# Optimization experiments

Measured on AMD Instinct MI355X. Metric: run time of the kernel, lower is better.

Reference implementation:

```python
import jax, jax.numpy as jnp
import numpy as np
from functools import partial

B, T, D, H, K = 4, 2048, 256, 8, 31
HD = D // H
EXP = 2  # FeedForward expansion
EPS = 1e-5


def setup_inputs() -> dict:
    key = jax.random.key(0)
    ks = iter(jax.random.split(key, 32))
    s = 0.02
    n = lambda shape: jax.random.normal(next(ks), shape, jnp.float32) * s
    ones = lambda shape: jnp.ones(shape, jnp.float32)
    zeros = lambda shape: jnp.zeros(shape, jnp.float32)
    return {
        "x": jax.random.normal(next(ks), (B, T, D), jnp.float32),
        # FF1
        "ff1_ln_g": ones((D,)), "ff1_ln_b": zeros((D,)),
        "ff1_w1": n((D, D * EXP)), "ff1_b1": zeros((D * EXP,)),
        "ff1_w2": n((D * EXP, D)), "ff1_b2": zeros((D,)),
        # MHSA
        "mhsa_ln_g": ones((D,)), "mhsa_ln_b": zeros((D,)),
        "qkv_w": n((D, 3 * D)), "qkv_b": zeros((3 * D,)),
        "out_w": n((D, D)), "out_b": zeros((D,)),
        # Conv module
        "conv_ln_g": ones((D,)), "conv_ln_b": zeros((D,)),
        "pw1_w": n((D, 2 * D)), "pw1_b": zeros((2 * D,)),
        "dw_w": n((D, 1, K)), "dw_b": zeros((D,)),
        "bn_g": ones((D,)), "bn_b": zeros((D,)),
        "pw2_w": n((D, D)), "pw2_b": zeros((D,)),
        # FF2
        "ff2_ln_g": ones((D,)), "ff2_ln_b": zeros((D,)),
        "ff2_w1": n((D, D * EXP)), "ff2_b1": zeros((D * EXP,)),
        "ff2_w2": n((D * EXP, D)), "ff2_b2": zeros((D,)),
        # Final LN
        "final_ln_g": ones((D,)), "final_ln_b": zeros((D,)),
    }


def layer_norm(x, g, b):
    mu = jnp.mean(x, axis=-1, keepdims=True)
    var = jnp.mean(jnp.square(x - mu), axis=-1, keepdims=True)
    return (x - mu) * jax.lax.rsqrt(var + EPS) * g + b


def feed_forward(x, ln_g, ln_b, w1, b1, w2, b2):
    h = layer_norm(x, ln_g, ln_b)
    h = jax.nn.silu(h @ w1 + b1)
    h = h @ w2 + b2
    return x + 0.5 * h


def mhsa(x, ln_g, ln_b, qkv_w, qkv_b, out_w, out_b):
    Bc, Tc, C = x.shape
    h = layer_norm(x, ln_g, ln_b)
    qkv = (h @ qkv_w + qkv_b).reshape(Bc, Tc, 3, H, HD)
    qkv = jnp.transpose(qkv, (2, 0, 3, 1, 4))  # [3,B,H,T,hd]
    q, k, v = qkv[0], qkv[1], qkv[2]
    attn = jnp.einsum("bhqd,bhkd->bhqk", q, k) / jnp.sqrt(jnp.float32(HD))
    attn = jax.nn.softmax(attn, axis=-1)
    out = jnp.einsum("bhqk,bhkd->bhqd", attn, v)
    out = jnp.transpose(out, (0, 2, 1, 3)).reshape(Bc, Tc, C)
    return x + (out @ out_w + out_b)


def conv_module(x, ln_g, ln_b, pw1_w, pw1_b, dw_w, dw_b, bn_g, bn_b, pw2_w, pw2_b):
    h = layer_norm(x, ln_g, ln_b)
    h = h @ pw1_w + pw1_b                      # [B,T,2D]
    a, g = jnp.split(h, 2, axis=-1)
    h = a * jax.nn.sigmoid(g)                  # GLU -> [B,T,D]
    h = jnp.transpose(h, (0, 2, 1))            # [B,D,T]
    h = jax.lax.conv_general_dilated(
        h, dw_w, window_strides=(1,), padding=[(K // 2, K // 2)],
        dimension_numbers=("NCH", "OIH", "NCH"), feature_group_count=D,
    ) + dw_b[None, :, None]
    # BatchNorm1d (training-mode batch stats, biased variance) over (B,T) per channel
    mu = jnp.mean(h, axis=(0, 2), keepdims=True)
    var = jnp.mean(jnp.square(h - mu), axis=(0, 2), keepdims=True)
    h = (h - mu) * jax.lax.rsqrt(var + EPS)
    h = h * bn_g[None, :, None] + bn_b[None, :, None]
    h = jax.nn.silu(h)
    h = jnp.transpose(h, (0, 2, 1))            # [B,T,D]
    h = h @ pw2_w + pw2_b
    return x + h


def reference(x,
              ff1_ln_g, ff1_ln_b, ff1_w1, ff1_b1, ff1_w2, ff1_b2,
              mhsa_ln_g, mhsa_ln_b, qkv_w, qkv_b, out_w, out_b,
              conv_ln_g, conv_ln_b, pw1_w, pw1_b, dw_w, dw_b, bn_g, bn_b,
              pw2_w, pw2_b,
              ff2_ln_g, ff2_ln_b, ff2_w1, ff2_b1, ff2_w2, ff2_b2,
              final_ln_g, final_ln_b):
    x = feed_forward(x, ff1_ln_g, ff1_ln_b, ff1_w1, ff1_b1, ff1_w2, ff1_b2)
    x = mhsa(x, mhsa_ln_g, mhsa_ln_b, qkv_w, qkv_b, out_w, out_b)
    x = conv_module(x, conv_ln_g, conv_ln_b, pw1_w, pw1_b, dw_w, dw_b,
                    bn_g, bn_b, pw2_w, pw2_b)
    x = feed_forward(x, ff2_ln_g, ff2_ln_b, ff2_w1, ff2_b1, ff2_w2, ff2_b2)
    return layer_norm(x, final_ln_g, final_ln_b)
```

## Files before the change

kernel.cpp:

```cpp
#include <hip/hip_runtime.h>
#include <hip/hip_bf16.h>

#define Bn 4
#define Tn 2048
#define Dn 256
#define Hn 8
#define HDn 32
#define KW 31
#define EPSV 1e-5f
#define NTOK (Bn * Tn)

typedef __attribute__((ext_vector_type(8))) short bf16x8;
typedef __attribute__((ext_vector_type(4))) float f32x4;
typedef unsigned short ushort_t;

__device__ __forceinline__ float sigmoidf_(float x) { return 1.f / (1.f + __expf(-x)); }
__device__ __forceinline__ unsigned short f2bfu(float f) {
    __hip_bfloat16 h = __float2bfloat16(f);
    unsigned short u; __builtin_memcpy(&u, &h, 2); return u;
}

template <int OUTBF>
__global__ __launch_bounds__(256) void ln_kernel(const float* __restrict__ x,
                                                 const float* __restrict__ g,
                                                 const float* __restrict__ b,
                                                 void* __restrict__ yp)
{
    const int row  = blockIdx.x * 4 + (threadIdx.x >> 6);
    const int lane = threadIdx.x & 63;
    const float* xr = x + (size_t)row * Dn + lane * 4;
    float4 v = *(const float4*)xr;
    float s = v.x + v.y + v.z + v.w;
#pragma unroll
    for (int o = 32; o > 0; o >>= 1) s += __shfl_xor(s, o, 64);
    const float mu = s * (1.f / Dn);
    const float dx = v.x - mu, dy = v.y - mu, dz = v.z - mu, dw = v.w - mu;
    float ss = dx * dx + dy * dy + dz * dz + dw * dw;
#pragma unroll
    for (int o = 32; o > 0; o >>= 1) ss += __shfl_xor(ss, o, 64);
    const float rstd = rsqrtf(ss * (1.f / Dn) + EPSV);
    const float4 gv = *(const float4*)(g + lane * 4);
    const float4 bv = *(const float4*)(b + lane * 4);
    float o0 = dx * rstd * gv.x + bv.x;
    float o1 = dy * rstd * gv.y + bv.y;
    float o2 = dz * rstd * gv.z + bv.z;
    float o3 = dw * rstd * gv.w + bv.w;
    if (OUTBF) {
        ushort4 o4;
        o4.x = f2bfu(o0); o4.y = f2bfu(o1); o4.z = f2bfu(o2); o4.w = f2bfu(o3);
        *(ushort4*)((ushort_t*)yp + (size_t)row * Dn + lane * 4) = o4;
    } else {
        float4 o4 = {o0, o1, o2, o3};
        *(float4*)((float*)yp + (size_t)row * Dn + lane * 4) = o4;
    }
}

struct WP {
    const float* s[8];
    unsigned     off[8];
    int          Kd[8];
    int          Nd[8];
};

__global__ __launch_bounds__(256) void wprep_kernel(WP p, ushort_t* __restrict__ wb)
{
    const int z = blockIdx.z;
    const int N = p.Nd[z], K = p.Kd[z];
    const int n0 = blockIdx.x * 64, k0 = blockIdx.y * 32;
    if (n0 >= N || k0 >= K) return;
    const float* src = p.s[z];
    ushort_t* dst = wb + p.off[z];
    const int nl = threadIdx.x & 63, kq = threadIdx.x >> 6;
    const int n = n0 + nl;
    const int kb = k0 + kq * 8;
    bf16x8 o;
#pragma unroll
    for (int i = 0; i < 8; ++i) o[i] = (short)f2bfu(src[(size_t)(kb + i) * N + n]);
    *(bf16x8*)(dst + (size_t)n * K + kb) = o;
}

template <int EPI>
__global__ __launch_bounds__(256) void bgemm_kernel(const ushort_t* __restrict__ A,
                                                    const ushort_t* __restrict__ Bt,
                                                    const float* __restrict__ bias,
                                                    const float* __restrict__ res,
                                                    void* __restrict__ Cp,
                                                    int N, int K, float scale)
{
    __shared__ ushort_t Af[8][64][8];
    __shared__ ushort_t Bf[8][64][8];
    const int tid = threadIdx.x;
    const int w   = tid >> 6;
    const int l   = tid & 63;
    const int g   = l >> 4;
    const int q16 = l & 15;
    const int wm  = w >> 1;
    const int wn  = w & 1;
    const int row0 = blockIdx.x * 128;
    const int col0 = blockIdx.y * 128;

    const ushort_t* ga0 = A  + (size_t)(row0 + (2 * w + 0) * 16 + q16) * K + g * 8;
    const ushort_t* ga1 = A  + (size_t)(row0 + (2 * w + 1) * 16 + q16) * K + g * 8;
    const ushort_t* gb0 = Bt + (size_t)(col0 + (2 * w + 0) * 16 + q16) * K + g * 8;
    const ushort_t* gb1 = Bt + (size_t)(col0 + (2 * w + 1) * 16 + q16) * K + g * 8;

    f32x4 acc[4][4];
#pragma unroll
    for (int mt = 0; mt < 4; ++mt)
#pragma unroll
        for (int nt = 0; nt < 4; ++nt) { acc[mt][nt].x = 0.f; acc[mt][nt].y = 0.f; acc[mt][nt].z = 0.f; acc[mt][nt].w = 0.f; }

    bf16x8 sa0 = *(const bf16x8*)ga0;
    bf16x8 sa1 = *(const bf16x8*)ga1;
    bf16x8 sb0 = *(const bf16x8*)gb0;
    bf16x8 sb1 = *(const bf16x8*)gb1;

    const int NKT = K >> 5;
    for (int kt = 0; kt < NKT; ++kt) {
        __syncthreads();
        *(bf16x8*)&Af[2 * w + 0][l][0] = sa0;
        *(bf16x8*)&Af[2 * w + 1][l][0] = sa1;
        *(bf16x8*)&Bf[2 * w + 0][l][0] = sb0;
        *(bf16x8*)&Bf[2 * w + 1][l][0] = sb1;
        if (kt + 1 < NKT) {
            const int k = (kt + 1) * 32;
            sa0 = *(const bf16x8*)(ga0 + k);
            sa1 = *(const bf16x8*)(ga1 + k);
            sb0 = *(const bf16x8*)(gb0 + k);
            sb1 = *(const bf16x8*)(gb1 + k);
        }
        __syncthreads();
        bf16x8 af[4], bb[4];
#pragma unroll
        for (int mt = 0; mt < 4; ++mt) af[mt] = *(const bf16x8*)&Af[wm * 4 + mt][l][0];
#pragma unroll
        for (int nt = 0; nt < 4; ++nt) bb[nt] = *(const bf16x8*)&Bf[wn * 4 + nt][l][0];
#pragma unroll
        for (int mt = 0; mt < 4; ++mt)
#pragma unroll
            for (int nt = 0; nt < 4; ++nt)
                acc[mt][nt] = __builtin_amdgcn_mfma_f32_16x16x32_bf16(af[mt], bb[nt], acc[mt][nt], 0, 0, 0);
    }

#pragma unroll
    for (int nt = 0; nt < 4; ++nt) {
        const int col = col0 + (wn * 4 + nt) * 16 + q16;
        const float bj = bias[col];
#pragma unroll
        for (int mt = 0; mt < 4; ++mt) {
            const int rowb = row0 + (wm * 4 + mt) * 16 + g * 4;
#pragma unroll
            for (int r = 0; r < 4; ++r) {
                float v = acc[mt][nt][r] + bj;
                const size_t idx = (size_t)(rowb + r) * N + col;
                if (EPI == 1) v *= sigmoidf_(v);
                if (EPI == 0 || EPI == 1) {
                    ((ushort_t*)Cp)[idx] = f2bfu(v);
                } else if (EPI == 2) {
                    ((float*)Cp)[idx] = res[idx] + scale * v;
                } else {
                    ((float*)Cp)[idx] = v;
                }
            }
        }
    }
}

__global__ __launch_bounds__(256) void attn_mfma_kernel(const ushort_t* __restrict__ qkv,
                                                        ushort_t* __restrict__ out)
{
    __shared__ ushort_t Kl[64][40];
    __shared__ ushort_t Vt[32][72];
    __shared__ ushort_t Pl[4][16][72];

    const int tid = threadIdx.x;
    const int w   = tid >> 6;
    const int l   = tid & 63;
    const int g   = l >> 4;
    const int q16 = l & 15;
    const int b   = blockIdx.y >> 3;
    const int h   = blockIdx.y & 7;
    const int q0  = blockIdx.x * 128 + w * 32;
    const ushort_t* base = qkv + (size_t)b * Tn * 768;

    bf16x8 qf[2];
#pragma unroll
    for (int u = 0; u < 2; ++u)
        qf[u] = *(const bf16x8*)(base + (size_t)(q0 + u * 16 + q16) * 768 + h * 32 + g * 8);

    f32x4 O[2][2];
    float mrun[2][4], lrun[2][4];
#pragma unroll
    for (int u = 0; u < 2; ++u)
#pragma unroll
        for (int t = 0; t < 2; ++t) { O[u][t].x = 0.f; O[u][t].y = 0.f; O[u][t].z = 0.f; O[u][t].w = 0.f; }
#pragma unroll
    for (int u = 0; u < 2; ++u)
#pragma unroll
        for (int r = 0; r < 4; ++r) { mrun[u][r] = 0.f; lrun[u][r] = 0.f; }

    const float cs = 0.25505392367033404f;

    const int kvr = tid >> 2;
    const int dsg = (tid & 3) * 8;

    for (int c0 = 0; c0 < Tn; c0 += 64) {
        __syncthreads();
        {
            const ushort_t* kp = base + (size_t)(c0 + kvr) * 768 + 256 + h * 32 + dsg;
            bf16x8 kk = *(const bf16x8*)kp;
            bf16x8 vv = *(const bf16x8*)(kp + 256);
            *(bf16x8*)&Kl[kvr][dsg] = kk;
            const int vcol = kvr ^ (dsg << 1);
#pragma unroll
            for (int i = 0; i < 8; ++i) Vt[dsg + i][vcol] = (ushort_t)vv[i];
        }
        __syncthreads();

        bf16x8 kb[4];
#pragma unroll
        for (int t = 0; t < 4; ++t)
            kb[t] = *(const bf16x8*)&Kl[t * 16 + q16][g * 8];
        bf16x8 vb[2][2];
#pragma unroll
        for (int ht = 0; ht < 2; ++ht) {
            const int d = ht * 16 + q16;
#pragma unroll
            for (int c = 0; c < 2; ++c)
                vb[ht][c] = *(const bf16x8*)&Vt[d][(c * 32 + g * 8) ^ ((d & 24) << 1)];
        }

#pragma unroll
        for (int u = 0; u < 2; ++u) {
            float p[4][4];
#pragma unroll
            for (int t = 0; t < 4; ++t) {
                f32x4 z = {0.f, 0.f, 0.f, 0.f};
                f32x4 s = __builtin_amdgcn_mfma_f32_16x16x32_bf16(qf[u], kb[t], z, 0, 0, 0);
#pragma unroll
                for (int r = 0; r < 4; ++r) p[t][r] = s[r] * cs;
            }
            float mx[4];
#pragma unroll
            for (int r = 0; r < 4; ++r)
                mx[r] = fmaxf(fmaxf(p[0][r], p[1][r]), fmaxf(p[2][r], p[3][r]));
#pragma unroll
            for (int o = 1; o < 16; o <<= 1)
#pragma unroll
                for (int r = 0; r < 4; ++r) mx[r] = fmaxf(mx[r], __shfl_xor(mx[r], o, 64));
            float wg = mx[0] - mrun[u][0];
#pragma unroll
            for (int r = 1; r < 4; ++r) wg = fmaxf(wg, mx[r] - mrun[u][r]);
            if (__any(wg > 11.f)) {
#pragma unroll
                for (int r = 0; r < 4; ++r) {
                    const float mn = fmaxf(mrun[u][r], mx[r]);
                    const float f  = exp2f(mrun[u][r] - mn);
                    lrun[u][r] *= f;
                    O[u][0][r] *= f;
                    O[u][1][r] *= f;
                    mrun[u][r] = mn;
                }
            }
#pragma unroll
            for (int t = 0; t < 4; ++t)
#pragma unroll
                for (int r = 0; r < 4; ++r) {
                    const float pe = exp2f(p[t][r] - mrun[u][r]);
                    lrun[u][r] += pe;
                    Pl[w][g * 4 + r][(t * 16 + q16) ^ (g << 4)] = f2bfu(pe);
                }
            bf16x8 pa[2];
#pragma unroll
            for (int c = 0; c < 2; ++c)
                pa[c] = *(const bf16x8*)&Pl[w][q16][(c * 32 + g * 8) ^ ((q16 >> 2) << 4)];
#pragma unroll
            for (int ht = 0; ht < 2; ++ht) {
                O[u][ht] = __builtin_amdgcn_mfma_f32_16x16x32_bf16(pa[0], vb[ht][0], O[u][ht], 0, 0, 0);
                O[u][ht] = __builtin_amdgcn_mfma_f32_16x16x32_bf16(pa[1], vb[ht][1], O[u][ht], 0, 0, 0);
            }
        }
    }

#pragma unroll
    for (int u = 0; u < 2; ++u) {
#pragma unroll
        for (int o = 1; o < 16; o <<= 1)
#pragma unroll
            for (int r = 0; r < 4; ++r) lrun[u][r] += __shfl_xor(lrun[u][r], o, 64);
#pragma unroll
        for (int r = 0; r < 4; ++r) {
            const float inv = 1.f / lrun[u][r];
            const int row = b * Tn + q0 + u * 16 + g * 4 + r;
#pragma unroll
            for (int ht = 0; ht < 2; ++ht)
                out[(size_t)row * Dn + h * 32 + ht * 16 + q16] = f2bfu(O[u][ht][r] * inv);
        }
    }
}

__global__ __launch_bounds__(256) void glu_kernel(const float* __restrict__ h,
                                                  float* __restrict__ outp)
{
    const size_t i   = (size_t)blockIdx.x * 256 + threadIdx.x;
    const size_t row = i / (Dn / 4);
    const int    c4  = (int)(i % (Dn / 4)) * 4;
    const float* hp  = h + row * (2 * Dn);
    const float4 a = *(const float4*)(hp + c4);
    const float4 g = *(const float4*)(hp + Dn + c4);
    float4 r;
    r.x = a.x * sigmoidf_(g.x);
    r.y = a.y * sigmoidf_(g.y);
    r.z = a.z * sigmoidf_(g.z);
    r.w = a.w * sigmoidf_(g.w);
    *(float4*)(outp + row * Dn + c4) = r;
}

__global__ __launch_bounds__(256) void dwconv_kernel(const float* __restrict__ in,
                                                     const float* __restrict__ w,
                                                     const float* __restrict__ wb,
                                                     float* __restrict__ outp)
{
    const int d  = threadIdx.x;
    const int b  = blockIdx.y;
    const int t0 = blockIdx.x * 8;
    float wr[KW];
#pragma unroll
    for (int k = 0; k < KW; ++k) wr[k] = w[d * KW + k];
    const float bias = wb[d];
    const float* bin  = in + (size_t)b * Tn * Dn + d;
    float* bout       = outp + (size_t)b * Tn * Dn + d;
    if (t0 >= (KW / 2) + 1 && t0 + 8 + KW / 2 <= Tn) {
        for (int i = 0; i < 8; ++i) {
            const int t = t0 + i;
            float s = bias;
#pragma unroll
            for (int k = 0; k < KW; ++k) s = fmaf(bin[(size_t)(t + k - KW / 2) * Dn], wr[k], s);
            bout[(size_t)t * Dn] = s;
        }
    } else {
        for (int i = 0; i < 8; ++i) {
            const int t = t0 + i;
            float s = bias;
#pragma unroll
            for (int k = 0; k < KW; ++k) {
                const int tt = t + k - KW / 2;
                if (tt >= 0 && tt < Tn) s = fmaf(bin[(size_t)tt * Dn], wr[k], s);
            }
            bout[(size_t)t * Dn] = s;
        }
    }
}

__global__ __launch_bounds__(256) void bnpart_kernel(const float* __restrict__ in,
                                                     float* __restrict__ part)
{
    const int d  = threadIdx.x;
    const int bk = blockIdx.x;
    float s = 0.f, ss = 0.f;
    const float* p = in + (size_t)bk * 32 * Dn + d;
    for (int t = 0; t < 32; ++t) {
        const float v = p[(size_t)t * Dn];
        s += v;
        ss = fmaf(v, v, ss);
    }
    part[bk * 512 + d]       = s;
    part[bk * 512 + 256 + d] = ss;
}

__global__ __launch_bounds__(256) void bnfin_kernel(const float* __restrict__ part,
                                                    float* __restrict__ meanp,
                                                    float* __restrict__ rstdp)
{
    const int d = threadIdx.x;
    float s = 0.f, ss = 0.f;
    for (int k = 0; k < 256; ++k) {
        s  += part[k * 512 + d];
        ss += part[k * 512 + 256 + d];
    }
    const float mu  = s * (1.f / NTOK);
    const float var = ss * (1.f / NTOK) - mu * mu;
    meanp[d] = mu;
    rstdp[d] = rsqrtf(var + EPSV);
}

__global__ __launch_bounds__(256) void bnsilu_kernel(const float* __restrict__ in,
                                                     const float* __restrict__ meanp,
                                                     const float* __restrict__ rstdp,
                                                     const float* __restrict__ g,
                                                     const float* __restrict__ bb,
                                                     ushort_t* __restrict__ outp)
{
    const size_t idx = ((size_t)blockIdx.x * 256 + threadIdx.x) * 4;
    const int d = (int)(idx & (Dn - 1));
    const float4 v = *(const float4*)(in + idx);
    ushort4 r;
    {
        float t;
        t = (v.x - meanp[d + 0]) * rstdp[d + 0] * g[d + 0] + bb[d + 0]; r.x = f2bfu(t * sigmoidf_(t));
        t = (v.y - meanp[d + 1]) * rstdp[d + 1] * g[d + 1] + bb[d + 1]; r.y = f2bfu(t * sigmoidf_(t));
        t = (v.z - meanp[d + 2]) * rstdp[d + 2] * g[d + 2] + bb[d + 2]; r.z = f2bfu(t * sigmoidf_(t));
        t = (v.w - meanp[d + 3]) * rstdp[d + 3] * g[d + 3] + bb[d + 3]; r.w = f2bfu(t * sigmoidf_(t));
    }
    *(ushort4*)(outp + idx) = r;
}

extern "C" void kernel_launch(void* const* d_in, const int* in_sizes, int n_in,
                              void* d_out, int out_size, void* d_ws, size_t ws_size,
                              hipStream_t stream)
{
    const float* x         = (const float*)d_in[0];
    const float* ff1_ln_g  = (const float*)d_in[1];
    const float* ff1_ln_b  = (const float*)d_in[2];
    const float* ff1_w1    = (const float*)d_in[3];
    const float* ff1_b1    = (const float*)d_in[4];
    const float* ff1_w2    = (const float*)d_in[5];
    const float* ff1_b2    = (const float*)d_in[6];
    const float* mhsa_ln_g = (const float*)d_in[7];
    const float* mhsa_ln_b = (const float*)d_in[8];
    const float* qkv_w     = (const float*)d_in[9];
    const float* qkv_b     = (const float*)d_in[10];
    const float* out_w     = (const float*)d_in[11];
    const float* out_b     = (const float*)d_in[12];
    const float* conv_ln_g = (const float*)d_in[13];
    const float* conv_ln_b = (const float*)d_in[14];
    const float* pw1_w     = (const float*)d_in[15];
    const float* pw1_b     = (const float*)d_in[16];
    const float* dw_w      = (const float*)d_in[17];
    const float* dw_b      = (const float*)d_in[18];
    const float* bn_g      = (const float*)d_in[19];
    const float* bn_b      = (const float*)d_in[20];
    const float* pw2_w     = (const float*)d_in[21];
    const float* pw2_b     = (const float*)d_in[22];
    const float* ff2_ln_g  = (const float*)d_in[23];
    const float* ff2_ln_b  = (const float*)d_in[24];
    const float* ff2_w1    = (const float*)d_in[25];
    const float* ff2_b1    = (const float*)d_in[26];
    const float* ff2_w2    = (const float*)d_in[27];
    const float* ff2_b2    = (const float*)d_in[28];
    const float* fin_ln_g  = (const float*)d_in[29];
    const float* fin_ln_b  = (const float*)d_in[30];

    char* W = (char*)d_ws;
    const size_t MB = 1u << 20;
    float*    R     = (float*)W;
    ushort_t* NbBF  = (ushort_t*)(W + 8 * MB);
    ushort_t* HBF   = (ushort_t*)(W + 12 * MB);
    float*    Hf32  = (float*)(W + 12 * MB);
    float*    Cb    = (float*)(W + 12 * MB);
    ushort_t* AtBF  = (ushort_t*)(W + 24 * MB);
    float*    part  = (float*)(W + 28 * MB);
    float*    meanp = part + 131072;
    float*    rstdp = meanp + 256;
    ushort_t* wbuf  = (ushort_t*)(W + 29 * MB);

    ushort_t* qkvT = wbuf;
    ushort_t* outT = wbuf + 196608;
    ushort_t* f11T = wbuf + 262144;
    ushort_t* f12T = wbuf + 393216;
    ushort_t* f21T = wbuf + 524288;
    ushort_t* f22T = wbuf + 655360;
    ushort_t* pw1T = wbuf + 786432;
    ushort_t* pw2T = wbuf + 917504;

    const dim3 blk(256);

    WP wp;
    wp.s[0] = qkv_w;  wp.off[0] = 0;      wp.Kd[0] = 256; wp.Nd[0] = 768;
    wp.s[1] = out_w;  wp.off[1] = 196608; wp.Kd[1] = 256; wp.Nd[1] = 256;
    wp.s[2] = ff1_w1; wp.off[2] = 262144; wp.Kd[2] = 256; wp.Nd[2] = 512;
    wp.s[3] = ff1_w2; wp.off[3] = 393216; wp.Kd[3] = 512; wp.Nd[3] = 256;
    wp.s[4] = ff2_w1; wp.off[4] = 524288; wp.Kd[4] = 256; wp.Nd[4] = 512;
    wp.s[5] = ff2_w2; wp.off[5] = 655360; wp.Kd[5] = 512; wp.Nd[5] = 256;
    wp.s[6] = pw1_w;  wp.off[6] = 786432; wp.Kd[6] = 256; wp.Nd[6] = 512;
    wp.s[7] = pw2_w;  wp.off[7] = 917504; wp.Kd[7] = 256; wp.Nd[7] = 256;
    wprep_kernel<<<dim3(12, 16, 8), blk, 0, stream>>>(wp, wbuf);

    ln_kernel<1><<<NTOK / 4, blk, 0, stream>>>(x, ff1_ln_g, ff1_ln_b, NbBF);
    bgemm_kernel<1><<<dim3(64, 4), blk, 0, stream>>>(NbBF, f11T, ff1_b1, nullptr, HBF, 512, 256, 0.f);
    bgemm_kernel<2><<<dim3(64, 2), blk, 0, stream>>>(HBF, f12T, ff1_b2, x, R, 256, 512, 0.5f);

    ln_kernel<1><<<NTOK / 4, blk, 0, stream>>>(R, mhsa_ln_g, mhsa_ln_b, NbBF);
    bgemm_kernel<0><<<dim3(64, 6), blk, 0, stream>>>(NbBF, qkvT, qkv_b, nullptr, HBF, 768, 256, 0.f);
    attn_mfma_kernel<<<dim3(16, 32), blk, 0, stream>>>(HBF, AtBF);
    bgemm_kernel<2><<<dim3(64, 2), blk, 0, stream>>>(AtBF, outT, out_b, R, R, 256, 256, 1.f);

    ln_kernel<1><<<NTOK / 4, blk, 0, stream>>>(R, conv_ln_g, conv_ln_b, NbBF);
    bgemm_kernel<3><<<dim3(64, 4), blk, 0, stream>>>(NbBF, pw1T, pw1_b, nullptr, Hf32, 512, 256, 0.f);
    glu_kernel<<<NTOK * Dn / 4 / 256, blk, 0, stream>>>(Hf32, (float*)d_out);
    dwconv_kernel<<<dim3(Tn / 8, Bn), blk, 0, stream>>>((float*)d_out, dw_w, dw_b, Cb);
    bnpart_kernel<<<256, blk, 0, stream>>>(Cb, part);
    bnfin_kernel<<<1, blk, 0, stream>>>(part, meanp, rstdp);
    bnsilu_kernel<<<NTOK * Dn / 4 / 256, blk, 0, stream>>>(Cb, meanp, rstdp, bn_g, bn_b, AtBF);
    bgemm_kernel<2><<<dim3(64, 2), blk, 0, stream>>>(AtBF, pw2T, pw2_b, R, R, 256, 256, 1.f);

    ln_kernel<1><<<NTOK / 4, blk, 0, stream>>>(R, ff2_ln_g, ff2_ln_b, NbBF);
    bgemm_kernel<1><<<dim3(64, 4), blk, 0, stream>>>(NbBF, f21T, ff2_b1, nullptr, HBF, 512, 256, 0.f);
    bgemm_kernel<2><<<dim3(64, 2), blk, 0, stream>>>(HBF, f22T, ff2_b2, R, R, 256, 512, 0.5f);

    ln_kernel<0><<<NTOK / 4, blk, 0, stream>>>(R, fin_ln_g, fin_ln_b, d_out);
}
```

Measured before the change: 392.8 us.

## Shrink GEMM tiles, per-wave K/V staging in attention, lazy softmax max

```diff
diff --git a/kernel.cpp b/kernel.cpp
--- a/kernel.cpp
+++ b/kernel.cpp
@@ -79,7 +79,7 @@
     *(bf16x8*)(dst + (size_t)n * K + kb) = o;
 }
 
-template <int EPI>
+template <int EPI, int BM>
 __global__ __launch_bounds__(256) void bgemm_kernel(const ushort_t* __restrict__ A,
                                                     const ushort_t* __restrict__ Bt,
                                                     const float* __restrict__ bias,
@@ -87,8 +87,11 @@
                                                     void* __restrict__ Cp,
                                                     int N, int K, float scale)
 {
-    __shared__ ushort_t Af[8][64][8];
-    __shared__ ushort_t Bf[8][64][8];
+    constexpr int ABLK = BM / 16;
+    constexpr int AST  = ABLK / 4;
+    constexpr int MT   = BM / 32;
+    __shared__ ushort_t Af[ABLK][64][8];
+    __shared__ ushort_t Bf[4][64][8];
     const int tid = threadIdx.x;
     const int w   = tid >> 6;
     const int l   = tid & 63;
@@ -96,59 +99,59 @@
     const int q16 = l & 15;
     const int wm  = w >> 1;
     const int wn  = w & 1;
-    const int row0 = blockIdx.x * 128;
-    const int col0 = blockIdx.y * 128;
-
-    const ushort_t* ga0 = A  + (size_t)(row0 + (2 * w + 0) * 16 + q16) * K + g * 8;
-    const ushort_t* ga1 = A  + (size_t)(row0 + (2 * w + 1) * 16 + q16) * K + g * 8;
-    const ushort_t* gb0 = Bt + (size_t)(col0 + (2 * w + 0) * 16 + q16) * K + g * 8;
-    const ushort_t* gb1 = Bt + (size_t)(col0 + (2 * w + 1) * 16 + q16) * K + g * 8;
-
-    f32x4 acc[4][4];
-#pragma unroll
-    for (int mt = 0; mt < 4; ++mt)
-#pragma unroll
-        for (int nt = 0; nt < 4; ++nt) { acc[mt][nt].x = 0.f; acc[mt][nt].y = 0.f; acc[mt][nt].z = 0.f; acc[mt][nt].w = 0.f; }
-
-    bf16x8 sa0 = *(const bf16x8*)ga0;
-    bf16x8 sa1 = *(const bf16x8*)ga1;
-    bf16x8 sb0 = *(const bf16x8*)gb0;
-    bf16x8 sb1 = *(const bf16x8*)gb1;
+    const int row0 = blockIdx.x * BM;
+    const int col0 = blockIdx.y * 64;
+    const int sbi  = tid >> 6;
+
+    const ushort_t* ga[AST];
+#pragma unroll
+    for (int i = 0; i < AST; ++i)
+        ga[i] = A + (size_t)(row0 + (sbi + 4 * i) * 16 + q16) * K + g * 8;
+    const ushort_t* gb = Bt + (size_t)(col0 + sbi * 16 + q16) * K + g * 8;
+
+    f32x4 acc[MT][2];
+#pragma unroll
+    for (int mt = 0; mt < MT; ++mt)
+#pragma unroll
+        for (int nt = 0; nt < 2; ++nt) { acc[mt][nt].x = 0.f; acc[mt][nt].y = 0.f; acc[mt][nt].z = 0.f; acc[mt][nt].w = 0.f; }
+
+    bf16x8 sa[AST], sb;
+#pragma unroll
+    for (int i = 0; i < AST; ++i) sa[i] = *(const bf16x8*)ga[i];
+    sb = *(const bf16x8*)gb;
 
     const int NKT = K >> 5;
     for (int kt = 0; kt < NKT; ++kt) {
         __syncthreads();
-        *(bf16x8*)&Af[2 * w + 0][l][0] = sa0;
-        *(bf16x8*)&Af[2 * w + 1][l][0] = sa1;
-        *(bf16x8*)&Bf[2 * w + 0][l][0] = sb0;
-        *(bf16x8*)&Bf[2 * w + 1][l][0] = sb1;
+#pragma unroll
+        for (int i = 0; i < AST; ++i) *(bf16x8*)&Af[sbi + 4 * i][l][0] = sa[i];
+        *(bf16x8*)&Bf[sbi][l][0] = sb;
         if (kt + 1 < NKT) {
             const int k = (kt + 1) * 32;
-            sa0 = *(const bf16x8*)(ga0 + k);
-            sa1 = *(const bf16x8*)(ga1 + k);
-            sb0 = *(const bf16x8*)(gb0 + k);
-            sb1 = *(const bf16x8*)(gb1 + k);
+#pragma unroll
+            for (int i = 0; i < AST; ++i) sa[i] = *(const bf16x8*)(ga[i] + k);
+            sb = *(const bf16x8*)(gb + k);
         }
         __syncthreads();
-        bf16x8 af[4], bb[4];
-#pragma unroll
-        for (int mt = 0; mt < 4; ++mt) af[mt] = *(const bf16x8*)&Af[wm * 4 + mt][l][0];
-#pragma unroll
-        for (int nt = 0; nt < 4; ++nt) bb[nt] = *(const bf16x8*)&Bf[wn * 4 + nt][l][0];
-#pragma unroll
-        for (int mt = 0; mt < 4; ++mt)
-#pragma unroll
-            for (int nt = 0; nt < 4; ++nt)
+        bf16x8 af[MT], bb[2];
+#pragma unroll
+        for (int mt = 0; mt < MT; ++mt) af[mt] = *(const bf16x8*)&Af[wm * MT + mt][l][0];
+#pragma unroll
+        for (int nt = 0; nt < 2; ++nt) bb[nt] = *(const bf16x8*)&Bf[wn * 2 + nt][l][0];
+#pragma unroll
+        for (int mt = 0; mt < MT; ++mt)
+#pragma unroll
+            for (int nt = 0; nt < 2; ++nt)
                 acc[mt][nt] = __builtin_amdgcn_mfma_f32_16x16x32_bf16(af[mt], bb[nt], acc[mt][nt], 0, 0, 0);
     }
 
 #pragma unroll
-    for (int nt = 0; nt < 4; ++nt) {
-        const int col = col0 + (wn * 4 + nt) * 16 + q16;
+    for (int nt = 0; nt < 2; ++nt) {
+        const int col = col0 + (wn * 2 + nt) * 16 + q16;
         const float bj = bias[col];
 #pragma unroll
-        for (int mt = 0; mt < 4; ++mt) {
-            const int rowb = row0 + (wm * 4 + mt) * 16 + g * 4;
+        for (int mt = 0; mt < MT; ++mt) {
+            const int rowb = row0 + (wm * MT + mt) * 16 + g * 4;
 #pragma unroll
             for (int r = 0; r < 4; ++r) {
                 float v = acc[mt][nt][r] + bj;
@@ -169,8 +172,8 @@
 __global__ __launch_bounds__(256) void attn_mfma_kernel(const ushort_t* __restrict__ qkv,
                                                         ushort_t* __restrict__ out)
 {
-    __shared__ ushort_t Kl[64][40];
-    __shared__ ushort_t Vt[32][72];
+    __shared__ ushort_t Kl[4][64][40];
+    __shared__ ushort_t Vt[4][32][72];
     __shared__ ushort_t Pl[4][16][72];
 
     const int tid = threadIdx.x;
@@ -201,33 +204,45 @@
 
     const float cs = 0.25505392367033404f;
 
-    const int kvr = tid >> 2;
-    const int dsg = (tid & 3) * 8;
+    const ushort_t* kvp = base + (size_t)l * 768 + 256 + h * 32;
+    bf16x8 nk[4], nv[4];
+#pragma unroll
+    for (int j = 0; j < 4; ++j) {
+        nk[j] = *(const bf16x8*)(kvp + j * 8);
+        nv[j] = *(const bf16x8*)(kvp + 256 + j * 8);
+    }
 
     for (int c0 = 0; c0 < Tn; c0 += 64) {
-        __syncthreads();
-        {
-            const ushort_t* kp = base + (size_t)(c0 + kvr) * 768 + 256 + h * 32 + dsg;
-            bf16x8 kk = *(const bf16x8*)kp;
-            bf16x8 vv = *(const bf16x8*)(kp + 256);
-            *(bf16x8*)&Kl[kvr][dsg] = kk;
-            const int vcol = kvr ^ (dsg << 1);
-#pragma unroll
-            for (int i = 0; i < 8; ++i) Vt[dsg + i][vcol] = (ushort_t)vv[i];
-        }
-        __syncthreads();
+#pragma unroll
+        for (int j = 0; j < 4; ++j)
+            *(bf16x8*)&Kl[w][l][j * 8] = nk[j];
+#pragma unroll
+        for (int j = 0; j < 4; ++j) {
+            const int vcol = l ^ (16 * j);
+#pragma unroll
+            for (int i = 0; i < 8; ++i)
+                Vt[w][j * 8 + i][vcol] = (ushort_t)nv[j][i];
+        }
+        if (c0 + 64 < Tn) {
+            const ushort_t* np = kvp + (size_t)(c0 + 64) * 768;
+#pragma unroll
+            for (int j = 0; j < 4; ++j) {
+                nk[j] = *(const bf16x8*)(np + j * 8);
+                nv[j] = *(const bf16x8*)(np + 256 + j * 8);
+            }
+        }
 
         bf16x8 kb[4];
 #pragma unroll
         for (int t = 0; t < 4; ++t)
-            kb[t] = *(const bf16x8*)&Kl[t * 16 + q16][g * 8];
+            kb[t] = *(const bf16x8*)&Kl[w][t * 16 + q16][g * 8];
         bf16x8 vb[2][2];
 #pragma unroll
         for (int ht = 0; ht < 2; ++ht) {
             const int d = ht * 16 + q16;
 #pragma unroll
             for (int c = 0; c < 2; ++c)
-                vb[ht][c] = *(const bf16x8*)&Vt[d][(c * 32 + g * 8) ^ ((d & 24) << 1)];
+                vb[ht][c] = *(const bf16x8*)&Vt[w][d][(c * 32 + g * 8) ^ ((d & 24) << 1)];
         }
 
 #pragma unroll
@@ -240,18 +255,20 @@
 #pragma unroll
                 for (int r = 0; r < 4; ++r) p[t][r] = s[r] * cs;
             }
-            float mx[4];
-#pragma unroll
-            for (int r = 0; r < 4; ++r)
-                mx[r] = fmaxf(fmaxf(p[0][r], p[1][r]), fmaxf(p[2][r], p[3][r]));
-#pragma unroll
-            for (int o = 1; o < 16; o <<= 1)
-#pragma unroll
-                for (int r = 0; r < 4; ++r) mx[r] = fmaxf(mx[r], __shfl_xor(mx[r], o, 64));
-            float wg = mx[0] - mrun[u][0];
-#pragma unroll
-            for (int r = 1; r < 4; ++r) wg = fmaxf(wg, mx[r] - mrun[u][r]);
-            if (__any(wg > 11.f)) {
+            float wgl = p[0][0] - mrun[u][0];
+#pragma unroll
+            for (int t = 0; t < 4; ++t)
+#pragma unroll
+                for (int r = 0; r < 4; ++r) wgl = fmaxf(wgl, p[t][r] - mrun[u][r]);
+            if (__builtin_expect(__any(wgl > 11.f) != 0, 0)) {
+                float mx[4];
+#pragma unroll
+                for (int r = 0; r < 4; ++r)
+                    mx[r] = fmaxf(fmaxf(p[0][r], p[1][r]), fmaxf(p[2][r], p[3][r]));
+#pragma unroll
+                for (int o = 1; o < 16; o <<= 1)
+#pragma unroll
+                    for (int r = 0; r < 4; ++r) mx[r] = fmaxf(mx[r], __shfl_xor(mx[r], o, 64));
 #pragma unroll
                 for (int r = 0; r < 4; ++r) {
                     const float mn = fmaxf(mrun[u][r], mx[r]);
@@ -477,26 +494,26 @@
     wprep_kernel<<<dim3(12, 16, 8), blk, 0, stream>>>(wp, wbuf);
 
     ln_kernel<1><<<NTOK / 4, blk, 0, stream>>>(x, ff1_ln_g, ff1_ln_b, NbBF);
-    bgemm_kernel<1><<<dim3(64, 4), blk, 0, stream>>>(NbBF, f11T, ff1_b1, nullptr, HBF, 512, 256, 0.f);
-    bgemm_kernel<2><<<dim3(64, 2), blk, 0, stream>>>(HBF, f12T, ff1_b2, x, R, 256, 512, 0.5f);
+    bgemm_kernel<1, 128><<<dim3(64, 8), blk, 0, stream>>>(NbBF, f11T, ff1_b1, nullptr, HBF, 512, 256, 0.f);
+    bgemm_kernel<2, 64><<<dim3(128, 4), blk, 0, stream>>>(HBF, f12T, ff1_b2, x, R, 256, 512, 0.5f);
 
     ln_kernel<1><<<NTOK / 4, blk, 0, stream>>>(R, mhsa_ln_g, mhsa_ln_b, NbBF);
-    bgemm_kernel<0><<<dim3(64, 6), blk, 0, stream>>>(NbBF, qkvT, qkv_b, nullptr, HBF, 768, 256, 0.f);
+    bgemm_kernel<0, 128><<<dim3(64, 12), blk, 0, stream>>>(NbBF, qkvT, qkv_b, nullptr, HBF, 768, 256, 0.f);
     attn_mfma_kernel<<<dim3(16, 32), blk, 0, stream>>>(HBF, AtBF);
-    bgemm_kernel<2><<<dim3(64, 2), blk, 0, stream>>>(AtBF, outT, out_b, R, R, 256, 256, 1.f);
+    bgemm_kernel<2, 64><<<dim3(128, 4), blk, 0, stream>>>(AtBF, outT, out_b, R, R, 256, 256, 1.f);
 
     ln_kernel<1><<<NTOK / 4, blk, 0, stream>>>(R, conv_ln_g, conv_ln_b, NbBF);
-    bgemm_kernel<3><<<dim3(64, 4), blk, 0, stream>>>(NbBF, pw1T, pw1_b, nullptr, Hf32, 512, 256, 0.f);
+    bgemm_kernel<3, 128><<<dim3(64, 8), blk, 0, stream>>>(NbBF, pw1T, pw1_b, nullptr, Hf32, 512, 256, 0.f);
     glu_kernel<<<NTOK * Dn / 4 / 256, blk, 0, stream>>>(Hf32, (float*)d_out);
     dwconv_kernel<<<dim3(Tn / 8, Bn), blk, 0, stream>>>((float*)d_out, dw_w, dw_b, Cb);
     bnpart_kernel<<<256, blk, 0, stream>>>(Cb, part);
     bnfin_kernel<<<1, blk, 0, stream>>>(part, meanp, rstdp);
     bnsilu_kernel<<<NTOK * Dn / 4 / 256, blk, 0, stream>>>(Cb, meanp, rstdp, bn_g, bn_b, AtBF);
-    bgemm_kernel<2><<<dim3(64, 2), blk, 0, stream>>>(AtBF, pw2T, pw2_b, R, R, 256, 256, 1.f);
+    bgemm_kernel<2, 64><<<dim3(128, 4), blk, 0, stream>>>(AtBF, pw2T, pw2_b, R, R, 256, 256, 1.f);
 
     ln_kernel<1><<<NTOK / 4, blk, 0, stream>>>(R, ff2_ln_g, ff2_ln_b, NbBF);
-    bgemm_kernel<1><<<dim3(64, 4), blk, 0, stream>>>(NbBF, f21T, ff2_b1, nullptr, HBF, 512, 256, 0.f);
-    bgemm_kernel<2><<<dim3(64, 2), blk, 0, stream>>>(HBF, f22T, ff2_b2, R, R, 256, 512, 0.5f);
+    bgemm_kernel<1, 128><<<dim3(64, 8), blk, 0, stream>>>(NbBF, f21T, ff2_b1, nullptr, HBF, 512, 256, 0.f);
+    bgemm_kernel<2, 64><<<dim3(128, 4), blk, 0, stream>>>(HBF, f22T, ff2_b2, R, R, 256, 512, 0.5f);
 
     ln_kernel<0><<<NTOK / 4, blk, 0, stream>>>(R, fin_ln_g, fin_ln_b, d_out);
 }
```

After: 369.5 us. 1.06x faster.
